# Performance work log

Hardware: AMD Instinct MI355X
Metric: run time of the kernel (lower is better)

Reference implementation:

```python
import jax, jax.numpy as jnp
import numpy as np

B, T, C = 2, 2048, 1024
H = 16
D = C // H  # head_size = 64
EPS = 1e-5


def setup_inputs() -> dict:
    key = jax.random.key(0)
    ks = jax.random.split(key, 16)
    s = lambda fan_in: fan_in ** -0.5
    return {
        "x": jax.random.normal(ks[0], (B, T, C), jnp.float32),
        "Wq": jax.random.normal(ks[1], (H, C, D), jnp.float32) * s(C),
        "Wk": jax.random.normal(ks[2], (H, C, D), jnp.float32) * s(C),
        "Wv": jax.random.normal(ks[3], (H, C, D), jnp.float32) * s(C),
        "Wproj": jax.random.normal(ks[4], (C, C), jnp.float32) * s(C),
        "bproj": jnp.zeros((C,), jnp.float32),
        "W1": jax.random.normal(ks[5], (C, 4 * C), jnp.float32) * s(C),
        "b1": jnp.zeros((4 * C,), jnp.float32),
        "W2": jax.random.normal(ks[6], (4 * C, C), jnp.float32) * s(4 * C),
        "b2": jnp.zeros((C,), jnp.float32),
        "ln1_g": jnp.ones((C,), jnp.float32),
        "ln1_b": jnp.zeros((C,), jnp.float32),
        "ln2_g": jnp.ones((C,), jnp.float32),
        "ln2_b": jnp.zeros((C,), jnp.float32),
    }


def _layernorm(x, g, b):
    mu = jnp.mean(x, axis=-1, keepdims=True)
    var = jnp.mean(jnp.square(x - mu), axis=-1, keepdims=True)
    return (x - mu) * jax.lax.rsqrt(var + EPS) * g + b


def _block(x, Wq, Wk, Wv, Wproj, bproj, W1, b1, W2, b2,
           ln1_g, ln1_b, ln2_g, ln2_b):
    # --- multi-head causal self-attention (pre-LN) ---
    h = _layernorm(x, ln1_g, ln1_b)
    q = jnp.einsum("btc,hcd->bhtd", h, Wq)
    k = jnp.einsum("btc,hcd->bhtd", h, Wk)
    v = jnp.einsum("btc,hcd->bhtd", h, Wv)
    scores = jnp.einsum("bhtd,bhsd->bhts", q, k) * (D ** -0.5)  # [B,H,T,T]
    causal = jnp.tril(jnp.ones((T, T), bool))
    scores = jnp.where(causal, scores, -jnp.inf)
    att = jax.nn.softmax(scores, axis=-1)
    out = jnp.einsum("bhts,bhsd->bhtd", att, v)  # [B,H,T,D]
    out = out.transpose(0, 2, 1, 3).reshape(B, T, H * D)  # concat heads
    x = x + out @ Wproj + bproj
    # --- feed-forward ---
    h2 = _layernorm(x, ln2_g, ln2_b)
    ff = jax.nn.relu(h2 @ W1 + b1) @ W2 + b2
    return x + ff


def reference(x, Wq, Wk, Wv, Wproj, bproj, W1, b1, W2, b2,
              ln1_g, ln1_b, ln2_g, ln2_b):
    return _block(x, Wq, Wk, Wv, Wproj, bproj, W1, b1, W2, b2,
                  ln1_g, ln1_b, ln2_g, ln2_b)
```

## Files before the change

### kernel.cpp

```cpp
#include <hip/hip_runtime.h>

typedef __bf16 bf16x8 __attribute__((ext_vector_type(8)));
typedef float  f32x4  __attribute__((ext_vector_type(4)));

union U8 { bf16x8 v; __bf16 e[8]; unsigned short u[8]; };

__device__ __forceinline__ unsigned short f2bf(float f) {
  union { __bf16 b; unsigned short u; } c;
  c.b = (__bf16)f;
  return c.u;
}

__device__ __forceinline__ void async16(const void* g, void* l) {
  __builtin_amdgcn_global_load_lds(
      (__attribute__((address_space(1))) void*)(g),
      (__attribute__((address_space(3))) void*)(l), 16, 0, 0);
}

__device__ __forceinline__ void block_barrier() {
  asm volatile("" ::: "memory");
  __builtin_amdgcn_sched_barrier(0);
  __builtin_amdgcn_s_barrier();
  __builtin_amdgcn_sched_barrier(0);
  asm volatile("" ::: "memory");
}

__global__ __launch_bounds__(256) void transpose_w(
    const float* __restrict__ in, unsigned short* __restrict__ out,
    int R, int Cc) {
  __shared__ float tile[32][33];
  const int batch = blockIdx.z;
  const float* ip = in + (size_t)batch * R * Cc;
  unsigned short* op = out + (size_t)batch * R * Cc;
  const int c0 = blockIdx.x * 32, r0 = blockIdx.y * 32;
  const int tx = threadIdx.x, ty = threadIdx.y;
#pragma unroll
  for (int i = 0; i < 32; i += 8)
    tile[ty + i][tx] = ip[(size_t)(r0 + ty + i) * Cc + c0 + tx];
  __syncthreads();
#pragma unroll
  for (int i = 0; i < 32; i += 8)
    op[(size_t)(c0 + ty + i) * R + r0 + tx] = f2bf(tile[tx][ty + i]);
}

__global__ __launch_bounds__(256) void ln_kernel(
    const float* __restrict__ x, const float* __restrict__ g,
    const float* __restrict__ bta, unsigned short* __restrict__ out) {
  const int C = 1024;
  const int row = blockIdx.x, tid = threadIdx.x;
  const float4 v = ((const float4*)(x + (size_t)row * C))[tid];
  float s  = v.x + v.y + v.z + v.w;
  float ss = v.x * v.x + v.y * v.y + v.z * v.z + v.w * v.w;
#pragma unroll
  for (int off = 32; off > 0; off >>= 1) {
    s  += __shfl_down(s, off);
    ss += __shfl_down(ss, off);
  }
  __shared__ float r0[4], r1[4];
  const int wave = tid >> 6, lane = tid & 63;
  if (lane == 0) { r0[wave] = s; r1[wave] = ss; }
  __syncthreads();
  s  = r0[0] + r0[1] + r0[2] + r0[3];
  ss = r1[0] + r1[1] + r1[2] + r1[3];
  const float mu   = s * (1.0f / C);
  const float var  = ss * (1.0f / C) - mu * mu;
  const float rstd = rsqrtf(var + 1e-5f);
  const float4 gv = ((const float4*)g)[tid];
  const float4 bv = ((const float4*)bta)[tid];
  ushort4 o;
  o.x = f2bf((v.x - mu) * rstd * gv.x + bv.x);
  o.y = f2bf((v.y - mu) * rstd * gv.y + bv.y);
  o.z = f2bf((v.z - mu) * rstd * gv.z + bv.z);
  o.w = f2bf((v.w - mu) * rstd * gv.w + bv.w);
  ((ushort4*)(out + (size_t)row * C))[tid] = o;
}

__global__ __launch_bounds__(256, 2) void gemm_lat2(
    const unsigned short* __restrict__ A, const unsigned short* __restrict__ BT,
    float* __restrict__ Cout, const float* __restrict__ bias,
    const float* __restrict__ resid, int M, int N, int K) {
  __shared__ __align__(16) unsigned short As[3][8192];
  __shared__ __align__(16) unsigned short Bs[3][4096];
  const int tid = threadIdx.x;
  const int lane = tid & 63, wave = tid >> 6;
  const int wm = wave >> 1, wn = wave & 1;
  const int lr = lane & 15, lg = lane >> 4;

  const int nwg = gridDim.x;
  const int cpx = nwg >> 3;
  const int swz = ((int)blockIdx.x & 7) * cpx + ((int)blockIdx.x >> 3);
  const int Nt = N >> 6;
  const int g4 = swz / (4 * Nt);
  const int rem = swz - g4 * 4 * Nt;
  const int m0 = (g4 * 4 + (rem & 3)) << 7;
  const int n0 = (rem >> 2) << 6;

  const int srow = tid >> 3;
  const int sc = ((tid & 7) ^ (srow & 7)) << 3;
  const unsigned short* Ag = A + (size_t)(m0 + srow) * K + sc;
  const unsigned short* Bg = BT + (size_t)(n0 + srow) * K + sc;
  const size_t rskip = (size_t)32 * K;

  f32x4 acc[4][2] = {};
  const int nkt = K >> 6;

#define STG(T, B)                                                          \
  {                                                                        \
    const int kt_ = (T) << 6;                                              \
    _Pragma("unroll")                                                      \
    for (int j = 0; j < 4; ++j)                                            \
      async16(Ag + kt_ + (size_t)j * rskip, &As[B][j * 2048 + tid * 8]);   \
    async16(Bg + kt_, &Bs[B][tid * 8]);                                    \
    async16(Bg + kt_ + rskip, &Bs[B][2048 + tid * 8]);                     \
  }

  STG(0, 0);
  STG(1, 1);

  for (int t = 0; t < nkt; ++t) {
    const int buf = t % 3;
    if (t + 1 < nkt) asm volatile("s_waitcnt vmcnt(6)" ::: "memory");
    else             asm volatile("s_waitcnt vmcnt(0)" ::: "memory");
    block_barrier();
    if (t + 2 < nkt) {
      int sb = buf + 2; if (sb >= 3) sb -= 3;
      STG(t + 2, sb);
    }
#pragma unroll
    for (int kh = 0; kh < 2; ++kh) {
      const int kc = ((kh * 4 + lg) ^ (lr & 7)) << 3;
      bf16x8 afr[4], bfr[2];
#pragma unroll
      for (int fm = 0; fm < 4; fm++)
        afr[fm] = *(const bf16x8*)&As[buf][(wm * 64 + fm * 16 + lr) * 64 + kc];
#pragma unroll
      for (int fn = 0; fn < 2; fn++)
        bfr[fn] = *(const bf16x8*)&Bs[buf][(wn * 32 + fn * 16 + lr) * 64 + kc];
#pragma unroll
      for (int fm = 0; fm < 4; fm++)
#pragma unroll
        for (int fn = 0; fn < 2; fn++)
          acc[fm][fn] = __builtin_amdgcn_mfma_f32_16x16x32_bf16(
              afr[fm], bfr[fn], acc[fm][fn], 0, 0, 0);
    }
  }
#undef STG

#pragma unroll
  for (int fn = 0; fn < 2; fn++) {
    const int col = n0 + wn * 32 + fn * 16 + lr;
    const float bv = bias[col];
#pragma unroll
    for (int fm = 0; fm < 4; fm++) {
      const int row0 = m0 + wm * 64 + fm * 16 + lg * 4;
#pragma unroll
      for (int r = 0; r < 4; r++) {
        const size_t idx = (size_t)(row0 + r) * N + col;
        Cout[idx] = acc[fm][fn][r] + bv + resid[idx];
      }
    }
  }
}

__global__ __launch_bounds__(256) void reduce_add4(
    const unsigned short* __restrict__ p01, const unsigned short* __restrict__ p23,
    const float* __restrict__ bias, float* __restrict__ out, int n4) {
  const int stride = gridDim.x * 256;
#define BF(u) __uint_as_float(((unsigned)(u)) << 16)
  for (int i = blockIdx.x * 256 + threadIdx.x; i < n4; i += stride) {
    const ushort4 a = ((const ushort4*)p01)[i];
    const ushort4 b = ((const ushort4*)p01)[i + n4];
    const ushort4 c = ((const ushort4*)p23)[i];
    const ushort4 d = ((const ushort4*)p23)[i + n4];
    const float4 r = ((const float4*)out)[i];
    const float4 bv = ((const float4*)bias)[i & 255];
    float4 o;
    o.x = (BF(a.x) + BF(b.x)) + (BF(c.x) + BF(d.x)) + r.x + bv.x;
    o.y = (BF(a.y) + BF(b.y)) + (BF(c.y) + BF(d.y)) + r.y + bv.y;
    o.z = (BF(a.z) + BF(b.z)) + (BF(c.z) + BF(d.z)) + r.z + bv.z;
    o.w = (BF(a.w) + BF(b.w)) + (BF(c.w) + BF(d.w)) + r.w + bv.w;
    ((float4*)out)[i] = o;
  }
#undef BF
}

template <int EPI, int SPLITK>
__global__ __launch_bounds__(512, 2) void gemm8p(
    const unsigned short* __restrict__ A, const unsigned short* __restrict__ BT,
    void* __restrict__ Cout, void* __restrict__ Cout2,
    const float* __restrict__ bias, int M, int N, int K) {
  __shared__ __align__(16) unsigned short As[2][2][8192];
  __shared__ __align__(16) unsigned short Bs[2][2][8192];
  const int tid = threadIdx.x;
  const int lane = tid & 63;
  const int wave = tid >> 6;
  const int wm = wave >> 2, wn = wave & 3;
  const int lr = lane & 15, lg = lane >> 4;

  const int nwg = gridDim.x;
  const int cpx = nwg >> 3;
  const int swz = ((int)blockIdx.x & 7) * cpx + ((int)blockIdx.x >> 3);
  int tile = swz, ks = 0;
  if (SPLITK > 1) {
    const int tilesPer = nwg / SPLITK;
    ks = swz / tilesPer;
    tile = swz - ks * tilesPer;
  }
  const int Ksl = K / SPLITK;
  const int k0 = ks * Ksl;
  const int Nt = N >> 8;
  const int g4 = tile / (4 * Nt);
  const int rem = tile - g4 * 4 * Nt;
  const int m0 = (g4 * 4 + (rem & 3)) << 8;
  const int n0 = (rem >> 2) << 8;

  const int srow = tid >> 2;
  const int scg = ((tid & 3) ^ ((srow >> 1) & 3)) << 3;
  const unsigned short* Ag = A + (size_t)(m0 + srow) * K + k0 + scg;
  const unsigned short* Bg = BT + (size_t)(n0 + srow) * K + k0 + scg;
  const size_t rskip = (size_t)128 * K;
  const int l8 = tid * 8;

  const int kch = (lg ^ ((lr >> 1) & 3)) << 3;

  f32x4 acc[8][4] = {};
  bf16x8 afr[4], bfr[4];
  const int nkt = Ksl >> 6;

  async16(Ag, &As[0][0][l8]);            async16(Ag + rskip, &As[0][0][l8 + 4096]);
  async16(Bg, &Bs[0][0][l8]);            async16(Bg + rskip, &Bs[0][0][l8 + 4096]);
  async16(Ag + 32, &As[0][1][l8]);       async16(Ag + 32 + rskip, &As[0][1][l8 + 4096]);
  async16(Bg + 32, &Bs[0][1][l8]);       async16(Bg + 32 + rskip, &Bs[0][1][l8 + 4096]);
  async16(Ag + 64, &As[1][0][l8]);       async16(Ag + 64 + rskip, &As[1][0][l8 + 4096]);
  async16(Bg + 64, &Bs[1][0][l8]);       async16(Bg + 64 + rskip, &Bs[1][0][l8 + 4096]);
  asm volatile("s_waitcnt vmcnt(4)" ::: "memory");
  block_barrier();

  for (int t = 0; t < nkt; ++t) {
    const int buf = t & 1, nbuf = buf ^ 1;
    const int kt1 = (t + 1) << 6, kt2 = (t + 2) << 6;
    const bool s1 = (t + 1 < nkt), s2 = (t + 2 < nkt);

#pragma unroll
    for (int fm = 0; fm < 4; fm++)
      afr[fm] = *(const bf16x8*)&As[buf][0][(wm * 128 + fm * 16 + lr) * 32 + kch];
#pragma unroll
    for (int fn = 0; fn < 4; fn++)
      bfr[fn] = *(const bf16x8*)&Bs[buf][0][(wn * 64 + fn * 16 + lr) * 32 + kch];
    if (s1) {
      async16(Ag + kt1 + 32, &As[nbuf][1][l8]);
      async16(Ag + kt1 + 32 + rskip, &As[nbuf][1][l8 + 4096]);
    }
    block_barrier();
    __builtin_amdgcn_s_setprio(1);
#pragma unroll
    for (int fm = 0; fm < 4; fm++)
#pragma unroll
      for (int fn = 0; fn < 4; fn++)
        acc[fm][fn] = __builtin_amdgcn_mfma_f32_16x16x32_bf16(afr[fm], bfr[fn], acc[fm][fn], 0, 0, 0);
    __builtin_amdgcn_s_setprio(0);
    block_barrier();

#pragma unroll
    for (int fm = 0; fm < 4; fm++)
      afr[fm] = *(const bf16x8*)&As[buf][0][(wm * 128 + 64 + fm * 16 + lr) * 32 + kch];
    if (s1) {
      async16(Bg + kt1 + 32, &Bs[nbuf][1][l8]);
      async16(Bg + kt1 + 32 + rskip, &Bs[nbuf][1][l8 + 4096]);
    }
    block_barrier();
    __builtin_amdgcn_s_setprio(1);
#pragma unroll
    for (int fm = 0; fm < 4; fm++)
#pragma unroll
      for (int fn = 0; fn < 4; fn++)
        acc[4 + fm][fn] = __builtin_amdgcn_mfma_f32_16x16x32_bf16(afr[fm], bfr[fn], acc[4 + fm][fn], 0, 0, 0);
    __builtin_amdgcn_s_setprio(0);
    block_barrier();

#pragma unroll
    for (int fm = 0; fm < 4; fm++)
      afr[fm] = *(const bf16x8*)&As[buf][1][(wm * 128 + fm * 16 + lr) * 32 + kch];
#pragma unroll
    for (int fn = 0; fn < 4; fn++)
      bfr[fn] = *(const bf16x8*)&Bs[buf][1][(wn * 64 + fn * 16 + lr) * 32 + kch];
    if (s2) {
      async16(Ag + kt2, &As[buf][0][l8]);
      async16(Ag + kt2 + rskip, &As[buf][0][l8 + 4096]);
    }
    block_barrier();
    __builtin_amdgcn_s_setprio(1);
#pragma unroll
    for (int fm = 0; fm < 4; fm++)
#pragma unroll
      for (int fn = 0; fn < 4; fn++)
        acc[fm][fn] = __builtin_amdgcn_mfma_f32_16x16x32_bf16(afr[fm], bfr[fn], acc[fm][fn], 0, 0, 0);
    __builtin_amdgcn_s_setprio(0);
    block_barrier();

#pragma unroll
    for (int fm = 0; fm < 4; fm++)
      afr[fm] = *(const bf16x8*)&As[buf][1][(wm * 128 + 64 + fm * 16 + lr) * 32 + kch];
    if (s2) {
      async16(Bg + kt2, &Bs[buf][0][l8]);
      async16(Bg + kt2 + rskip, &Bs[buf][0][l8 + 4096]);
    }
    block_barrier();
    __builtin_amdgcn_s_setprio(1);
#pragma unroll
    for (int fm = 0; fm < 4; fm++)
#pragma unroll
      for (int fn = 0; fn < 4; fn++)
        acc[4 + fm][fn] = __builtin_amdgcn_mfma_f32_16x16x32_bf16(afr[fm], bfr[fn], acc[4 + fm][fn], 0, 0, 0);
    __builtin_amdgcn_s_setprio(0);
    if (s2) asm volatile("s_waitcnt vmcnt(4)" ::: "memory");
    else    asm volatile("s_waitcnt vmcnt(0)" ::: "memory");
    block_barrier();
  }

#pragma unroll
  for (int fn = 0; fn < 4; fn++) {
    const int col = n0 + wn * 64 + fn * 16 + lr;
    float bv = 0.0f;
    if (EPI == 2) bv = bias[col];
#pragma unroll
    for (int fm = 0; fm < 8; fm++) {
      const int row0 = m0 + wm * 128 + fm * 16 + lg * 4;
      if (EPI == 2) {
#pragma unroll
        for (int r = 0; r < 4; r++)
          ((unsigned short*)Cout)[(size_t)(row0 + r) * N + col] =
              f2bf(fmaxf(acc[fm][fn][r] + bv, 0.0f));
      } else if (EPI == 5) {
        unsigned short* P = (unsigned short*)(ks < 2 ? Cout : Cout2) +
                            (size_t)(ks & 1) * M * N;
#pragma unroll
        for (int r = 0; r < 4; r++)
          P[(size_t)(row0 + r) * N + col] = f2bf(acc[fm][fn][r]);
      } else {
        if (col < 2048) {
#pragma unroll
          for (int r = 0; r < 4; r++) {
            float val = acc[fm][fn][r];
            if (col < 1024) val *= 0.18033688011112042f;
            ((unsigned short*)Cout)[(size_t)(row0 + r) * 2048 + col] = f2bf(val);
          }
        } else {
          ushort4 ov;
          ov.x = f2bf(acc[fm][fn][0]);
          ov.y = f2bf(acc[fm][fn][1]);
          ov.z = f2bf(acc[fm][fn][2]);
          ov.w = f2bf(acc[fm][fn][3]);
          *(ushort4*)((unsigned short*)Cout2 + (size_t)(col - 2048) * 4096 + row0) = ov;
        }
      }
    }
  }
}

__global__ __launch_bounds__(256) void attn_kernel(
    const unsigned short* __restrict__ qk, const unsigned short* __restrict__ vT,
    unsigned short* __restrict__ o) {
  const int T = 2048, C = 1024, QKS = 2048;
  const int tid = threadIdx.x;
  const int wave = tid >> 6, lane = tid & 63;
  const int lr = lane & 15, lg = lane >> 4;

  const int id = (int)blockIdx.x;
  const int rest = id >> 3;
  const int qp = rest & 15;
  const int bhv = ((rest >> 4) << 3) | (id & 7);
  const int b = bhv >> 4, hh = bhv & 15;

  const size_t rowb = (size_t)b * T * QKS;
  const int qcol = hh * 64;
  const int kcol = 1024 + hh * 64;
  const int vrow0 = hh * 64;
  const size_t bT = (size_t)b * T;
  const int swe = (lr & 7) << 3;

  __shared__ __align__(16) unsigned short Ks[2][64 * 64];
  __shared__ __align__(16) unsigned short Vs[2][64 * 64];
  __shared__ __align__(16) unsigned short Ps[4][16][72];

  const int rw = tid >> 3;
  const int c8 = ((tid & 7) ^ (rw & 7)) << 3;

#pragma unroll 1
  for (int pass = 0; pass < 2; ++pass) {
    const int qt = (pass == 0) ? qp : (31 - qp);
    const int qbase = qt * 64 + wave * 16;
    const int trow = qbase + lr;

    U8 qf[2];
#pragma unroll
    for (int j = 0; j < 2; j++)
      qf[j].v = *(const bf16x8*)(qk + rowb + (size_t)trow * QKS + qcol + j * 32 + lg * 8);
    asm volatile("s_waitcnt vmcnt(0)" ::: "memory");

    async16(qk + rowb + (size_t)rw * QKS + kcol + c8, Ks[0] + tid * 8);
    async16(qk + rowb + (size_t)(32 + rw) * QKS + kcol + c8, Ks[0] + 2048 + tid * 8);
    async16(vT + (size_t)(vrow0 + rw) * 4096 + bT + c8, Vs[0] + tid * 8);
    async16(vT + (size_t)(vrow0 + 32 + rw) * 4096 + bT + c8, Vs[0] + 2048 + tid * 8);

    f32x4 oa[4] = {};
    float mrun = -1e30f, lsum = 0.0f;
    int cur = 0;

    for (int sb = 0; sb <= qt; ++sb) {
      if (sb < qt) {
        const int s1 = (sb + 1) * 64;
        const int nb = cur ^ 1;
        async16(qk + rowb + (size_t)(s1 + rw) * QKS + kcol + c8, Ks[nb] + tid * 8);
        async16(qk + rowb + (size_t)(s1 + 32 + rw) * QKS + kcol + c8, Ks[nb] + 2048 + tid * 8);
        async16(vT + (size_t)(vrow0 + rw) * 4096 + bT + s1 + c8, Vs[nb] + tid * 8);
        async16(vT + (size_t)(vrow0 + 32 + rw) * 4096 + bT + s1 + c8, Vs[nb] + 2048 + tid * 8);
        asm volatile("s_waitcnt vmcnt(4)" ::: "memory");
      } else {
        asm volatile("s_waitcnt vmcnt(0)" ::: "memory");
      }
      block_barrier();

      const unsigned short* Kc = Ks[cur];
      const unsigned short* Vc = Vs[cur];
      const int s0 = sb * 64;

      f32x4 sa[4] = {};
#pragma unroll
      for (int j = 0; j < 2; j++) {
#pragma unroll
        for (int mf = 0; mf < 4; mf++) {
          U8 kf;
          kf.v = *(const bf16x8*)(Kc + (mf * 16 + lr) * 64 + ((j * 32 + lg * 8) ^ swe));
          sa[mf] = __builtin_amdgcn_mfma_f32_16x16x32_bf16(kf.v, qf[j].v, sa[mf], 0, 0, 0);
        }
      }
      float sv[16];
#pragma unroll
      for (int mf = 0; mf < 4; mf++)
#pragma unroll
        for (int r = 0; r < 4; r++) sv[mf * 4 + r] = sa[mf][r];

      if (sb == qt) {
#pragma unroll
        for (int mf = 0; mf < 4; mf++)
#pragma unroll
          for (int r = 0; r < 4; r++)
            if (s0 + mf * 16 + lg * 4 + r > trow) sv[mf * 4 + r] = -1e30f;
      }

      float t8[8];
#pragma unroll
      for (int i = 0; i < 8; i++) t8[i] = fmaxf(sv[i], sv[i + 8]);
#pragma unroll
      for (int i = 0; i < 4; i++) t8[i] = fmaxf(t8[i], t8[i + 4]);
      float tm = fmaxf(fmaxf(t8[0], t8[1]), fmaxf(t8[2], t8[3]));
      tm = fmaxf(tm, __shfl_xor(tm, 16));
      tm = fmaxf(tm, __shfl_xor(tm, 32));

      if (!__all(tm <= mrun + 8.0f)) {
        const float mn = fmaxf(mrun, tm);
        const float corr = __builtin_amdgcn_exp2f(mrun - mn);
        lsum *= corr;
#pragma unroll
        for (int c = 0; c < 4; c++)
#pragma unroll
          for (int r = 0; r < 4; r++) oa[c][r] *= corr;
        mrun = mn;
      }

#pragma unroll
      for (int i = 0; i < 16; i++)
        sv[i] = __builtin_amdgcn_exp2f(sv[i] - mrun);
      float s8[8];
#pragma unroll
      for (int i = 0; i < 8; i++) s8[i] = sv[i] + sv[i + 8];
#pragma unroll
      for (int i = 0; i < 4; i++) s8[i] = s8[i] + s8[i + 4];
      float rs = (s8[0] + s8[1]) + (s8[2] + s8[3]);
      rs += __shfl_xor(rs, 16);
      rs += __shfl_xor(rs, 32);
      lsum += rs;

#pragma unroll
      for (int mf = 0; mf < 4; mf++) {
        ushort4 w;
        w.x = f2bf(sv[mf * 4 + 0]);
        w.y = f2bf(sv[mf * 4 + 1]);
        w.z = f2bf(sv[mf * 4 + 2]);
        w.w = f2bf(sv[mf * 4 + 3]);
        *(ushort4*)&Ps[wave][lr][mf * 16 + lg * 4] = w;
      }
      asm volatile("" ::: "memory");
      U8 pb[2];
      pb[0].v = *(const bf16x8*)&Ps[wave][lr][lg * 8];
      pb[1].v = *(const bf16x8*)&Ps[wave][lr][32 + lg * 8];
      asm volatile("" ::: "memory");

#pragma unroll
      for (int c = 0; c < 4; c++) {
#pragma unroll
        for (int ks = 0; ks < 2; ks++) {
          U8 vf;
          vf.v = *(const bf16x8*)(Vc + (c * 16 + lr) * 64 + ((ks * 32 + lg * 8) ^ swe));
          oa[c] = __builtin_amdgcn_mfma_f32_16x16x32_bf16(vf.v, pb[ks].v, oa[c], 0, 0, 0);
        }
      }

      block_barrier();
      cur ^= 1;
    }

    const float inv = 1.0f / lsum;
#pragma unroll
    for (int c = 0; c < 4; c++) {
      ushort4 ov;
      ov.x = f2bf(oa[c][0] * inv);
      ov.y = f2bf(oa[c][1] * inv);
      ov.z = f2bf(oa[c][2] * inv);
      ov.w = f2bf(oa[c][3] * inv);
      *(ushort4*)(o + (size_t)(bT + trow) * C + hh * 64 + c * 16 + lg * 4) = ov;
    }
  }
}

extern "C" void kernel_launch(void* const* d_in, const int* in_sizes, int n_in,
                              void* d_out, int out_size, void* d_ws, size_t ws_size,
                              hipStream_t stream) {
  (void)in_sizes; (void)n_in; (void)out_size; (void)ws_size;
  const int T = 2048, C = 1024, M = 2 * T, C4 = 4 * C;

  const float* x     = (const float*)d_in[0];
  const float* Wq    = (const float*)d_in[1];
  const float* Wk    = (const float*)d_in[2];
  const float* Wv    = (const float*)d_in[3];
  const float* Wproj = (const float*)d_in[4];
  const float* bproj = (const float*)d_in[5];
  const float* W1    = (const float*)d_in[6];
  const float* b1    = (const float*)d_in[7];
  const float* W2    = (const float*)d_in[8];
  const float* b2    = (const float*)d_in[9];
  const float* ln1g  = (const float*)d_in[10];
  const float* ln1b  = (const float*)d_in[11];
  const float* ln2g  = (const float*)d_in[12];
  const float* ln2b  = (const float*)d_in[13];
  float* out = (float*)d_out;

  char* ws = (char*)d_ws;
  const size_t MBy = (size_t)1 << 20;
  unsigned short* WqkvT = (unsigned short*)(ws + 0 * MBy);
  unsigned short* WqT = WqkvT;
  unsigned short* WkT = WqkvT + 1024 * 1024;
  unsigned short* WvT = WqkvT + 2048 * 1024;
  unsigned short* WpT = (unsigned short*)(ws + 6 * MBy);
  unsigned short* W1T = (unsigned short*)(ws + 8 * MBy);
  unsigned short* W2T = (unsigned short*)(ws + 16 * MBy);
  unsigned short* h   = (unsigned short*)(ws + 24 * MBy);
  unsigned short* qkb = (unsigned short*)(ws + 32 * MBy);
  unsigned short* vTb = (unsigned short*)(ws + 48 * MBy);
  unsigned short* att = (unsigned short*)(ws + 56 * MBy);
  float* x1 = out;
  unsigned short* h2  = att;
  unsigned short* ff1 = h;
  unsigned short* ffP01 = (unsigned short*)(ws + 0 * MBy);
  unsigned short* ffP23 = (unsigned short*)(ws + 64 * MBy);

  const dim3 tb(32, 8);
  transpose_w<<<dim3(2, 32, 16), tb, 0, stream>>>(Wq, WqT, 1024, 64);
  transpose_w<<<dim3(2, 32, 16), tb, 0, stream>>>(Wk, WkT, 1024, 64);
  transpose_w<<<dim3(2, 32, 16), tb, 0, stream>>>(Wv, WvT, 1024, 64);
  transpose_w<<<dim3(32, 32, 1), tb, 0, stream>>>(Wproj, WpT, 1024, 1024);
  transpose_w<<<dim3(128, 32, 1), tb, 0, stream>>>(W1, W1T, 1024, 4096);
  transpose_w<<<dim3(32, 128, 1), tb, 0, stream>>>(W2, W2T, 4096, 1024);

  ln_kernel<<<M, 256, 0, stream>>>(x, ln1g, ln1b, h);

  gemm8p<4, 1><<<192, 512, 0, stream>>>(h, WqkvT, qkb, vTb, nullptr, M, 3072, C);

  attn_kernel<<<512, 256, 0, stream>>>(qkb, vTb, att);

  gemm_lat2<<<512, 256, 0, stream>>>(att, WpT, x1, bproj, x, M, C, C);

  ln_kernel<<<M, 256, 0, stream>>>(x1, ln2g, ln2b, h2);

  gemm8p<2, 1><<<256, 512, 0, stream>>>(h2, W1T, ff1, nullptr, b1, M, C4, C);

  gemm8p<5, 4><<<256, 512, 0, stream>>>(ff1, W2T, ffP01, ffP23, nullptr, M, C, C4);
  reduce_add4<<<2048, 256, 0, stream>>>(ffP01, ffP23, b2, out, M * C / 4);
}
```

Before: 238.1 us.

## Split paired attention passes into separate blocks, heaviest first; merge QKV transposes

The attention kernel drops the two-pass scheme, where each block handled a light and a heavy query tile for causal balance. It now launches one block per query tile, with block ids mapped so the longest tiles start first and the hardware scheduler does the balancing. It also adds a launch_bounds occupancy hint and raises wave priority around the MFMA sections. Separately, the three per-head Q/K/V weight transposes are merged into a single launch, saving two kernel launches at the cost of a select on the source pointer.

```diff
diff --git a/kernel.cpp b/kernel.cpp
--- a/kernel.cpp
+++ b/kernel.cpp
@@ -32,6 +32,27 @@
   const int batch = blockIdx.z;
   const float* ip = in + (size_t)batch * R * Cc;
   unsigned short* op = out + (size_t)batch * R * Cc;
+  const int c0 = blockIdx.x * 32, r0 = blockIdx.y * 32;
+  const int tx = threadIdx.x, ty = threadIdx.y;
+#pragma unroll
+  for (int i = 0; i < 32; i += 8)
+    tile[ty + i][tx] = ip[(size_t)(r0 + ty + i) * Cc + c0 + tx];
+  __syncthreads();
+#pragma unroll
+  for (int i = 0; i < 32; i += 8)
+    op[(size_t)(c0 + ty + i) * R + r0 + tx] = f2bf(tile[tx][ty + i]);
+}
+
+__global__ __launch_bounds__(256) void transpose_qkv(
+    const float* __restrict__ Wq, const float* __restrict__ Wk,
+    const float* __restrict__ Wv, unsigned short* __restrict__ out) {
+  __shared__ float tile[32][33];
+  const int z = blockIdx.z;
+  const float* src = (z < 16) ? Wq : (z < 32 ? Wk : Wv);
+  const int batch = z & 15;
+  const int R = 1024, Cc = 64;
+  const float* ip = src + (size_t)batch * R * Cc;
+  unsigned short* op = out + (size_t)z * R * Cc;
   const int c0 = blockIdx.x * 32, r0 = blockIdx.y * 32;
   const int tx = threadIdx.x, ty = threadIdx.y;
 #pragma unroll
@@ -358,7 +379,7 @@
   }
 }
 
-__global__ __launch_bounds__(256) void attn_kernel(
+__global__ __launch_bounds__(256, 3) void attn_kernel(
     const unsigned short* __restrict__ qk, const unsigned short* __restrict__ vT,
     unsigned short* __restrict__ o) {
   const int T = 2048, C = 1024, QKS = 2048;
@@ -368,9 +389,10 @@
 
   const int id = (int)blockIdx.x;
   const int rest = id >> 3;
-  const int qp = rest & 15;
-  const int bhv = ((rest >> 4) << 3) | (id & 7);
-  const int b = bhv >> 4, hh = bhv & 15;
+  const int bhHi = rest & 3;
+  const int qt = 31 - (rest >> 2);
+  const int bh = (bhHi << 3) | (id & 7);
+  const int b = bh >> 4, hh = bh & 15;
 
   const size_t rowb = (size_t)b * T * QKS;
   const int qcol = hh * 64;
@@ -386,141 +408,141 @@
   const int rw = tid >> 3;
   const int c8 = ((tid & 7) ^ (rw & 7)) << 3;
 
-#pragma unroll 1
-  for (int pass = 0; pass < 2; ++pass) {
-    const int qt = (pass == 0) ? qp : (31 - qp);
-    const int qbase = qt * 64 + wave * 16;
-    const int trow = qbase + lr;
-
-    U8 qf[2];
-#pragma unroll
-    for (int j = 0; j < 2; j++)
-      qf[j].v = *(const bf16x8*)(qk + rowb + (size_t)trow * QKS + qcol + j * 32 + lg * 8);
-    asm volatile("s_waitcnt vmcnt(0)" ::: "memory");
-
-    async16(qk + rowb + (size_t)rw * QKS + kcol + c8, Ks[0] + tid * 8);
-    async16(qk + rowb + (size_t)(32 + rw) * QKS + kcol + c8, Ks[0] + 2048 + tid * 8);
-    async16(vT + (size_t)(vrow0 + rw) * 4096 + bT + c8, Vs[0] + tid * 8);
-    async16(vT + (size_t)(vrow0 + 32 + rw) * 4096 + bT + c8, Vs[0] + 2048 + tid * 8);
-
-    f32x4 oa[4] = {};
-    float mrun = -1e30f, lsum = 0.0f;
-    int cur = 0;
-
-    for (int sb = 0; sb <= qt; ++sb) {
-      if (sb < qt) {
-        const int s1 = (sb + 1) * 64;
-        const int nb = cur ^ 1;
-        async16(qk + rowb + (size_t)(s1 + rw) * QKS + kcol + c8, Ks[nb] + tid * 8);
-        async16(qk + rowb + (size_t)(s1 + 32 + rw) * QKS + kcol + c8, Ks[nb] + 2048 + tid * 8);
-        async16(vT + (size_t)(vrow0 + rw) * 4096 + bT + s1 + c8, Vs[nb] + tid * 8);
-        async16(vT + (size_t)(vrow0 + 32 + rw) * 4096 + bT + s1 + c8, Vs[nb] + 2048 + tid * 8);
-        asm volatile("s_waitcnt vmcnt(4)" ::: "memory");
-      } else {
-        asm volatile("s_waitcnt vmcnt(0)" ::: "memory");
+  const int qbase = qt * 64 + wave * 16;
+  const int trow = qbase + lr;
+
+  U8 qf[2];
+#pragma unroll
+  for (int j = 0; j < 2; j++)
+    qf[j].v = *(const bf16x8*)(qk + rowb + (size_t)trow * QKS + qcol + j * 32 + lg * 8);
+  asm volatile("s_waitcnt vmcnt(0)" ::: "memory");
+
+  async16(qk + rowb + (size_t)rw * QKS + kcol + c8, Ks[0] + tid * 8);
+  async16(qk + rowb + (size_t)(32 + rw) * QKS + kcol + c8, Ks[0] + 2048 + tid * 8);
+  async16(vT + (size_t)(vrow0 + rw) * 4096 + bT + c8, Vs[0] + tid * 8);
+  async16(vT + (size_t)(vrow0 + 32 + rw) * 4096 + bT + c8, Vs[0] + 2048 + tid * 8);
+
+  f32x4 oa[4] = {};
+  float mrun = -1e30f, lsum = 0.0f;
+  int cur = 0;
+
+  for (int sb = 0; sb <= qt; ++sb) {
+    if (sb < qt) {
+      const int s1 = (sb + 1) * 64;
+      const int nb = cur ^ 1;
+      async16(qk + rowb + (size_t)(s1 + rw) * QKS + kcol + c8, Ks[nb] + tid * 8);
+      async16(qk + rowb + (size_t)(s1 + 32 + rw) * QKS + kcol + c8, Ks[nb] + 2048 + tid * 8);
+      async16(vT + (size_t)(vrow0 + rw) * 4096 + bT + s1 + c8, Vs[nb] + tid * 8);
+      async16(vT + (size_t)(vrow0 + 32 + rw) * 4096 + bT + s1 + c8, Vs[nb] + 2048 + tid * 8);
+      asm volatile("s_waitcnt vmcnt(4)" ::: "memory");
+    } else {
+      asm volatile("s_waitcnt vmcnt(0)" ::: "memory");
+    }
+    block_barrier();
+
+    const unsigned short* Kc = Ks[cur];
+    const unsigned short* Vc = Vs[cur];
+    const int s0 = sb * 64;
+
+    f32x4 sa[4] = {};
+    __builtin_amdgcn_s_setprio(1);
+#pragma unroll
+    for (int j = 0; j < 2; j++) {
+#pragma unroll
+      for (int mf = 0; mf < 4; mf++) {
+        U8 kf;
+        kf.v = *(const bf16x8*)(Kc + (mf * 16 + lr) * 64 + ((j * 32 + lg * 8) ^ swe));
+        sa[mf] = __builtin_amdgcn_mfma_f32_16x16x32_bf16(kf.v, qf[j].v, sa[mf], 0, 0, 0);
       }
-      block_barrier();
-
-      const unsigned short* Kc = Ks[cur];
-      const unsigned short* Vc = Vs[cur];
-      const int s0 = sb * 64;
-
-      f32x4 sa[4] = {};
-#pragma unroll
-      for (int j = 0; j < 2; j++) {
-#pragma unroll
-        for (int mf = 0; mf < 4; mf++) {
-          U8 kf;
-          kf.v = *(const bf16x8*)(Kc + (mf * 16 + lr) * 64 + ((j * 32 + lg * 8) ^ swe));
-          sa[mf] = __builtin_amdgcn_mfma_f32_16x16x32_bf16(kf.v, qf[j].v, sa[mf], 0, 0, 0);
-        }
+    }
+    __builtin_amdgcn_s_setprio(0);
+    float sv[16];
+#pragma unroll
+    for (int mf = 0; mf < 4; mf++)
+#pragma unroll
+      for (int r = 0; r < 4; r++) sv[mf * 4 + r] = sa[mf][r];
+
+    if (sb == qt) {
+#pragma unroll
+      for (int mf = 0; mf < 4; mf++)
+#pragma unroll
+        for (int r = 0; r < 4; r++)
+          if (s0 + mf * 16 + lg * 4 + r > trow) sv[mf * 4 + r] = -1e30f;
+    }
+
+    float t8[8];
+#pragma unroll
+    for (int i = 0; i < 8; i++) t8[i] = fmaxf(sv[i], sv[i + 8]);
+#pragma unroll
+    for (int i = 0; i < 4; i++) t8[i] = fmaxf(t8[i], t8[i + 4]);
+    float tm = fmaxf(fmaxf(t8[0], t8[1]), fmaxf(t8[2], t8[3]));
+    tm = fmaxf(tm, __shfl_xor(tm, 16));
+    tm = fmaxf(tm, __shfl_xor(tm, 32));
+
+    if (!__all(tm <= mrun + 8.0f)) {
+      const float mn = fmaxf(mrun, tm);
+      const float corr = __builtin_amdgcn_exp2f(mrun - mn);
+      lsum *= corr;
+#pragma unroll
+      for (int c = 0; c < 4; c++)
+#pragma unroll
+        for (int r = 0; r < 4; r++) oa[c][r] *= corr;
+      mrun = mn;
+    }
+
+#pragma unroll
+    for (int i = 0; i < 16; i++)
+      sv[i] = __builtin_amdgcn_exp2f(sv[i] - mrun);
+    float s8[8];
+#pragma unroll
+    for (int i = 0; i < 8; i++) s8[i] = sv[i] + sv[i + 8];
+#pragma unroll
+    for (int i = 0; i < 4; i++) s8[i] = s8[i] + s8[i + 4];
+    float rs = (s8[0] + s8[1]) + (s8[2] + s8[3]);
+    rs += __shfl_xor(rs, 16);
+    rs += __shfl_xor(rs, 32);
+    lsum += rs;
+
+#pragma unroll
+    for (int mf = 0; mf < 4; mf++) {
+      ushort4 w;
+      w.x = f2bf(sv[mf * 4 + 0]);
+      w.y = f2bf(sv[mf * 4 + 1]);
+      w.z = f2bf(sv[mf * 4 + 2]);
+      w.w = f2bf(sv[mf * 4 + 3]);
+      *(ushort4*)&Ps[wave][lr][mf * 16 + lg * 4] = w;
+    }
+    asm volatile("" ::: "memory");
+    U8 pb[2];
+    pb[0].v = *(const bf16x8*)&Ps[wave][lr][lg * 8];
+    pb[1].v = *(const bf16x8*)&Ps[wave][lr][32 + lg * 8];
+    asm volatile("" ::: "memory");
+
+    __builtin_amdgcn_s_setprio(1);
+#pragma unroll
+    for (int c = 0; c < 4; c++) {
+#pragma unroll
+      for (int ks = 0; ks < 2; ks++) {
+        U8 vf;
+        vf.v = *(const bf16x8*)(Vc + (c * 16 + lr) * 64 + ((ks * 32 + lg * 8) ^ swe));
+        oa[c] = __builtin_amdgcn_mfma_f32_16x16x32_bf16(vf.v, pb[ks].v, oa[c], 0, 0, 0);
       }
-      float sv[16];
-#pragma unroll
-      for (int mf = 0; mf < 4; mf++)
-#pragma unroll
-        for (int r = 0; r < 4; r++) sv[mf * 4 + r] = sa[mf][r];
-
-      if (sb == qt) {
-#pragma unroll
-        for (int mf = 0; mf < 4; mf++)
-#pragma unroll
-          for (int r = 0; r < 4; r++)
-            if (s0 + mf * 16 + lg * 4 + r > trow) sv[mf * 4 + r] = -1e30f;
-      }
-
-      float t8[8];
-#pragma unroll
-      for (int i = 0; i < 8; i++) t8[i] = fmaxf(sv[i], sv[i + 8]);
-#pragma unroll
-      for (int i = 0; i < 4; i++) t8[i] = fmaxf(t8[i], t8[i + 4]);
-      float tm = fmaxf(fmaxf(t8[0], t8[1]), fmaxf(t8[2], t8[3]));
-      tm = fmaxf(tm, __shfl_xor(tm, 16));
-      tm = fmaxf(tm, __shfl_xor(tm, 32));
-
-      if (!__all(tm <= mrun + 8.0f)) {
-        const float mn = fmaxf(mrun, tm);
-        const float corr = __builtin_amdgcn_exp2f(mrun - mn);
-        lsum *= corr;
-#pragma unroll
-        for (int c = 0; c < 4; c++)
-#pragma unroll
-          for (int r = 0; r < 4; r++) oa[c][r] *= corr;
-        mrun = mn;
-      }
-
-#pragma unroll
-      for (int i = 0; i < 16; i++)
-        sv[i] = __builtin_amdgcn_exp2f(sv[i] - mrun);
-      float s8[8];
-#pragma unroll
-      for (int i = 0; i < 8; i++) s8[i] = sv[i] + sv[i + 8];
-#pragma unroll
-      for (int i = 0; i < 4; i++) s8[i] = s8[i] + s8[i + 4];
-      float rs = (s8[0] + s8[1]) + (s8[2] + s8[3]);
-      rs += __shfl_xor(rs, 16);
-      rs += __shfl_xor(rs, 32);
-      lsum += rs;
-
-#pragma unroll
-      for (int mf = 0; mf < 4; mf++) {
-        ushort4 w;
-        w.x = f2bf(sv[mf * 4 + 0]);
-        w.y = f2bf(sv[mf * 4 + 1]);
-        w.z = f2bf(sv[mf * 4 + 2]);
-        w.w = f2bf(sv[mf * 4 + 3]);
-        *(ushort4*)&Ps[wave][lr][mf * 16 + lg * 4] = w;
-      }
-      asm volatile("" ::: "memory");
-      U8 pb[2];
-      pb[0].v = *(const bf16x8*)&Ps[wave][lr][lg * 8];
-      pb[1].v = *(const bf16x8*)&Ps[wave][lr][32 + lg * 8];
-      asm volatile("" ::: "memory");
-
-#pragma unroll
-      for (int c = 0; c < 4; c++) {
-#pragma unroll
-        for (int ks = 0; ks < 2; ks++) {
-          U8 vf;
-          vf.v = *(const bf16x8*)(Vc + (c * 16 + lr) * 64 + ((ks * 32 + lg * 8) ^ swe));
-          oa[c] = __builtin_amdgcn_mfma_f32_16x16x32_bf16(vf.v, pb[ks].v, oa[c], 0, 0, 0);
-        }
-      }
-
-      block_barrier();
-      cur ^= 1;
-    }
-
-    const float inv = 1.0f / lsum;
-#pragma unroll
-    for (int c = 0; c < 4; c++) {
-      ushort4 ov;
-      ov.x = f2bf(oa[c][0] * inv);
-      ov.y = f2bf(oa[c][1] * inv);
-      ov.z = f2bf(oa[c][2] * inv);
-      ov.w = f2bf(oa[c][3] * inv);
-      *(ushort4*)(o + (size_t)(bT + trow) * C + hh * 64 + c * 16 + lg * 4) = ov;
-    }
+    }
+    __builtin_amdgcn_s_setprio(0);
+
+    block_barrier();
+    cur ^= 1;
+  }
+
+  const float inv = 1.0f / lsum;
+#pragma unroll
+  for (int c = 0; c < 4; c++) {
+    ushort4 ov;
+    ov.x = f2bf(oa[c][0] * inv);
+    ov.y = f2bf(oa[c][1] * inv);
+    ov.z = f2bf(oa[c][2] * inv);
+    ov.w = f2bf(oa[c][3] * inv);
+    *(ushort4*)(o + (size_t)(bT + trow) * C + hh * 64 + c * 16 + lg * 4) = ov;
   }
 }
 
@@ -549,9 +571,6 @@
   char* ws = (char*)d_ws;
   const size_t MBy = (size_t)1 << 20;
   unsigned short* WqkvT = (unsigned short*)(ws + 0 * MBy);
-  unsigned short* WqT = WqkvT;
-  unsigned short* WkT = WqkvT + 1024 * 1024;
-  unsigned short* WvT = WqkvT + 2048 * 1024;
   unsigned short* WpT = (unsigned short*)(ws + 6 * MBy);
   unsigned short* W1T = (unsigned short*)(ws + 8 * MBy);
   unsigned short* W2T = (unsigned short*)(ws + 16 * MBy);
@@ -566,9 +585,7 @@
   unsigned short* ffP23 = (unsigned short*)(ws + 64 * MBy);
 
   const dim3 tb(32, 8);
-  transpose_w<<<dim3(2, 32, 16), tb, 0, stream>>>(Wq, WqT, 1024, 64);
-  transpose_w<<<dim3(2, 32, 16), tb, 0, stream>>>(Wk, WkT, 1024, 64);
-  transpose_w<<<dim3(2, 32, 16), tb, 0, stream>>>(Wv, WvT, 1024, 64);
+  transpose_qkv<<<dim3(2, 32, 48), tb, 0, stream>>>(Wq, Wk, Wv, WqkvT);
   transpose_w<<<dim3(32, 32, 1), tb, 0, stream>>>(Wproj, WpT, 1024, 1024);
   transpose_w<<<dim3(128, 32, 1), tb, 0, stream>>>(W1, W1T, 1024, 4096);
   transpose_w<<<dim3(32, 128, 1), tb, 0, stream>>>(W2, W2T, 4096, 1024);
@@ -577,7 +594,7 @@
 
   gemm8p<4, 1><<<192, 512, 0, stream>>>(h, WqkvT, qkb, vTb, nullptr, M, 3072, C);
 
-  attn_kernel<<<512, 256, 0, stream>>>(qkb, vTb, att);
+  attn_kernel<<<1024, 256, 0, stream>>>(qkb, vTb, att);
 
   gemm_lat2<<<512, 256, 0, stream>>>(att, WpT, x1, bproj, x, M, C, C);
 
```

Measured after the change: 228.8 us. -3.9%, faster.
